# Kernel optimization log

Hardware: AMD Instinct MI355X
Metric: run time of the kernel (lower is better)

The kernel has to match this reference:

```python
import jax, jax.numpy as jnp
import numpy as np

K = 16  # nsample for knn_point

def _bn(x, g, b):
    # inference-mode BatchNorm1d folded to per-channel affine (running stats 0/1)
    return x * g[None, :, None] + b[None, :, None]

def _knn(xyz, k):
    # xyz: [B,3,N] -> idx [B,N,k] of k nearest neighbors (squared L2)
    p = xyz.transpose(0, 2, 1)                                   # [B,N,3]
    sq = jnp.sum(p * p, axis=-1)                                 # [B,N]
    d = sq[:, :, None] + sq[:, None, :] - 2.0 * jnp.einsum('bnc,bmc->bnm', p, p)
    _, idx = jax.lax.top_k(-d, k)
    return idx

def _gather(hT, idx):
    # hT: [B,N,C], idx: [B,N,K] -> [B,N,K,C]
    return jax.vmap(lambda a, i: a[i])(hT, idx)

def setup_inputs():
    key = jax.random.key(0)
    ks = jax.random.split(key, 12)
    B, N, C = 16, 2048, 128
    def w(k, shape, fan):
        return jax.random.normal(k, shape, jnp.float32) * (1.0 / np.sqrt(fan))
    o = jnp.ones; z = jnp.zeros
    return {
        'points': jax.random.normal(ks[0], (B, 6, N), jnp.float32),
        'label': jax.random.uniform(ks[1], (B, 1, 16), jnp.float32),
        'We1': w(ks[2], (C, 6), 6), 'ge1': o(C), 'be1': z(C),
        'We2': w(ks[3], (C, C), C), 'ge2': o(C), 'be2': z(C),
        'W1': w(ks[4], (3, C, C), C), 'g1': o((3, C)), 'b1': z((3, C)),
        'W2': w(ks[5], (3, C, C), C), 'g2': o((3, C)), 'b2': z((3, C)),
        'Wf': w(ks[6], (1024, 3 * C), 3 * C), 'gf': o(1024), 'bf': z(1024),
        'Wl': w(ks[7], (64, 16), 16), 'gl': o(64), 'bl': z(64),
        'Wc1': w(ks[8], (512, 3136), 3136), 'bc1': z(512), 'gc1': o(512), 'bb1': z(512),
        'Wc2': w(ks[9], (256, 512), 512), 'bc2': z(256), 'gc2': o(256), 'bb2': z(256),
        'Wc3': w(ks[10], (50, 256), 256), 'bc3': z(50),
    }

def reference(points, label, We1, ge1, be1, We2, ge2, be2, W1, g1, b1, W2, g2, b2,
              Wf, gf, bf, Wl, gl, bl, Wc1, bc1, gc1, bb1, Wc2, bc2, gc2, bb2, Wc3, bc3):
    B, _, N = points.shape
    x = points[:, :6, :]
    xyz = x[:, :3, :]
    idx = _knn(xyz, K)                                            # [B,N,16]
    # input embedding: two conv1x1 + BN + ReLU
    h = jax.nn.relu(_bn(jnp.einsum('oc,bcn->bon', We1, x), ge1, be1))
    h = jax.nn.relu(_bn(jnp.einsum('oc,bcn->bon', We2, h), ge2, be2))
    xs = []
    for i in range(3):  # PVDSA_Res blocks (simplified: conv-BN-ReLU, kNN max-agg, conv-BN + residual)
        t = jax.nn.relu(_bn(jnp.einsum('oc,bcn->bon', W1[i], h), g1[i], b1[i]))
        nbr = _gather(t.transpose(0, 2, 1), idx)                  # [B,N,K,C]
        m = nbr.max(axis=2).transpose(0, 2, 1)                    # [B,C,N]
        h = jax.nn.relu(_bn(jnp.einsum('oc,bcn->bon', W2[i], m), g2[i], b2[i]) + h)
        xs.append(h)
    xcat = jnp.concatenate(xs, axis=1)                            # [B,384,N]
    xf = jax.nn.leaky_relu(_bn(jnp.einsum('oc,bcn->bon', Wf, xcat), gf, bf), 0.2)  # [B,1024,N]
    x_max = xf.max(axis=-1)                                       # [B,1024]
    x_avg = xf.mean(axis=-1)                                      # [B,1024]
    cls = jnp.broadcast_to(label.transpose(0, 2, 1), (B, 16, N))
    lab = jax.nn.leaky_relu(_bn(jnp.einsum('oc,bcn->bon', Wl, cls), gl, bl), 0.2)  # [B,64,N]
    glob = jnp.concatenate([
        jnp.broadcast_to(x_max[:, :, None], (B, 1024, N)),
        jnp.broadcast_to(x_avg[:, :, None], (B, 1024, N)),
        lab], axis=1)
    xa = jnp.concatenate([xf, glob], axis=1)                      # [B,3136,N]
    c = jax.nn.relu(_bn(jnp.einsum('oc,bcn->bon', Wc1, xa) + bc1[None, :, None], gc1, bb1))
    c = jax.nn.relu(_bn(jnp.einsum('oc,bcn->bon', Wc2, c) + bc2[None, :, None], gc2, bb2))
    out = jnp.einsum('oc,bcn->bon', Wc3, c) + bc3[None, :, None]  # [B,50,N]
    return out
```

## Files before the change

### kernel.cpp

```cpp
#include <hip/hip_runtime.h>
#include <cstdint>
#include <cstddef>

#define DEVINL __device__ __forceinline__

typedef float    f32x4 __attribute__((ext_vector_type(4)));
typedef _Float16 f16x8 __attribute__((ext_vector_type(8)));
typedef _Float16 f16x4 __attribute__((ext_vector_type(4)));

constexpr int BB = 16, NN = 2048, MM = 32768;

constexpr size_t OFF_WE1 = 0;
constexpr size_t OFF_WE2 = OFF_WE1 + 128 * 64 * 2;
constexpr size_t OFF_W1  = OFF_WE2 + 128 * 128 * 2;
constexpr size_t OFF_W2  = OFF_W1  + 3 * 128 * 128 * 2;
constexpr size_t OFF_WF  = OFF_W2  + 3 * 128 * 128 * 2;
constexpr size_t OFF_WC1 = OFF_WF  + 1024 * 384 * 2;
constexpr size_t OFF_WC2 = OFF_WC1 + 512 * 1024 * 2;
constexpr size_t OFF_WC3 = OFF_WC2 + 256 * 512 * 2;
constexpr size_t OFF_BC2 = OFF_WC3 + 128 * 256 * 2;
constexpr size_t OFF_BC3 = OFF_BC2 + 256 * 4;
constexpr size_t OFF_CVEC= OFF_BC3 + 128 * 4;
constexpr size_t OFF_PMAX= OFF_CVEC+ 16 * 512 * 4;
constexpr size_t OFF_PSUM= OFF_PMAX+ 16 * 8 * 1024 * 4;
constexpr size_t OFF_IDX = OFF_PSUM+ 16 * 8 * 1024 * 4;
constexpr size_t OFF_R1  = 8ull << 20;
constexpr size_t OFF_X0  = OFF_R1;
constexpr size_t OFF_HT  = OFF_R1 + (4ull  << 20);
constexpr size_t OFF_TT  = OFF_R1 + (12ull << 20);
constexpr size_t OFF_MT  = OFF_R1 + (20ull << 20);
constexpr size_t OFF_C1  = OFF_R1;
constexpr size_t OFF_XCAT= OFF_R1 + (32ull << 20);
constexpr size_t OFF_C2  = OFF_XCAT;
constexpr size_t OFF_XF  = OFF_XCAT + (24ull << 20);

__global__ __launch_bounds__(256) void fold_all_kernel(
    const float* We1, const float* ge1, const float* We2, const float* ge2,
    const float* W1,  const float* g1,  const float* W2,  const float* g2,
    const float* Wf,  const float* gf,  const float* Wc1, const float* gc1,
    const float* Wc2, const float* gc2, const float* Wc3,
    const float* gc2b, const float* bc2, const float* bb2, const float* bc3,
    const float* pts, char* ws)
{
    const int bid = blockIdx.x;
    const int tid = threadIdx.x;

    if (bid == 4704) {
        ((float*)(ws + OFF_BC2))[tid] = gc2b[tid] * bc2[tid] + bb2[tid];
        return;
    }
    if (bid == 4705) {
        if (tid < 128) ((float*)(ws + OFF_BC3))[tid] = (tid < 50) ? bc3[tid] : 0.f;
        return;
    }
    if (bid >= 4706) {
        int m = (bid - 4706) * 256 + tid;
        int b = m >> 11, n = m & 2047;
        const float* ps = pts + (size_t)b * 6 * 2048 + n;
        _Float16 tmp[64];
#pragma unroll
        for (int c = 0; c < 64; ++c) tmp[c] = (_Float16)0.f;
#pragma unroll
        for (int c = 0; c < 6; ++c) tmp[c] = (_Float16)ps[(size_t)c << 11];
        _Float16* dst = (_Float16*)(ws + OFF_X0) + (size_t)m * 64;
#pragma unroll
        for (int v = 0; v < 8; ++v) *(f16x8*)(dst + v * 8) = *(const f16x8*)(tmp + v * 8);
        return;
    }

    int id, base;
    if      (bid < 32)   { id = 0;  base = 0;    }
    else if (bid < 96)   { id = 1;  base = 32;   }
    else if (bid < 160)  { id = 2;  base = 96;   }
    else if (bid < 224)  { id = 3;  base = 160;  }
    else if (bid < 288)  { id = 4;  base = 224;  }
    else if (bid < 352)  { id = 5;  base = 288;  }
    else if (bid < 416)  { id = 6;  base = 352;  }
    else if (bid < 480)  { id = 7;  base = 416;  }
    else if (bid < 2016) { id = 8;  base = 480;  }
    else if (bid < 4064) { id = 9;  base = 2016; }
    else if (bid < 4576) { id = 10; base = 4064; }
    else                 { id = 11; base = 4576; }

    const float* src = nullptr; const float* g = nullptr; _Float16* dst = nullptr;
    int O = 0, K = 0, lds = 0, Kp = 0;
    switch (id) {
        case 0:  src = We1; g = ge1; O = 128; K = 6;    lds = 6;    Kp = 64;   dst = (_Float16*)(ws + OFF_WE1); break;
        case 1:  src = We2; g = ge2; O = 128; K = 128;  lds = 128;  Kp = 128;  dst = (_Float16*)(ws + OFF_WE2); break;
        case 2: case 3: case 4: {
            int i = id - 2;
            src = W1 + (size_t)i * 16384; g = g1 + i * 128; O = 128; K = 128; lds = 128; Kp = 128;
            dst = (_Float16*)(ws + OFF_W1) + (size_t)i * 16384; break; }
        case 5: case 6: case 7: {
            int i = id - 5;
            src = W2 + (size_t)i * 16384; g = g2 + i * 128; O = 128; K = 128; lds = 128; Kp = 128;
            dst = (_Float16*)(ws + OFF_W2) + (size_t)i * 16384; break; }
        case 8:  src = Wf;  g = gf;  O = 1024; K = 384;  lds = 384;  Kp = 384;  dst = (_Float16*)(ws + OFF_WF);  break;
        case 9:  src = Wc1; g = gc1; O = 512;  K = 1024; lds = 3136; Kp = 1024; dst = (_Float16*)(ws + OFF_WC1); break;
        case 10: src = Wc2; g = gc2; O = 256;  K = 512;  lds = 512;  Kp = 512;  dst = (_Float16*)(ws + OFF_WC2); break;
        default: src = Wc3; g = nullptr; O = 50; K = 256; lds = 256; Kp = 256;  dst = (_Float16*)(ws + OFF_WC3); break;
    }
    int e = (bid - base) * 256 + tid;
    int o = e / Kp, k = e - o * Kp;
    float v = 0.f;
    if (o < O && k < K) {
        v = src[(size_t)o * lds + k];
        if (g) v *= g[o];
    }
    dst[e] = (_Float16)v;
}

DEVINL float knn_dist(const float4 pq, const float4 pm) {
    float t = pq.x * pm.x;
    t = fmaf(pq.y, pm.y, t);
    t = fmaf(pq.z, pm.z, t);
    return fmaf(-2.f, t, pm.w);
}

#define KNN_DINS(X) do { \
    const float x_ = (X); \
    d15 = __builtin_amdgcn_fmed3f(x_, d14, d15); \
    d14 = __builtin_amdgcn_fmed3f(x_, d13, d14); \
    d13 = __builtin_amdgcn_fmed3f(x_, d12, d13); \
    d12 = __builtin_amdgcn_fmed3f(x_, d11, d12); \
    d11 = __builtin_amdgcn_fmed3f(x_, d10, d11); \
    d10 = __builtin_amdgcn_fmed3f(x_, d9,  d10); \
    d9  = __builtin_amdgcn_fmed3f(x_, d8,  d9);  \
    d8  = __builtin_amdgcn_fmed3f(x_, d7,  d8);  \
    d7  = __builtin_amdgcn_fmed3f(x_, d6,  d7);  \
    d6  = __builtin_amdgcn_fmed3f(x_, d5,  d6);  \
    d5  = __builtin_amdgcn_fmed3f(x_, d4,  d5);  \
    d4  = __builtin_amdgcn_fmed3f(x_, d3,  d4);  \
    d3  = __builtin_amdgcn_fmed3f(x_, d2,  d3);  \
    d2  = __builtin_amdgcn_fmed3f(x_, d1,  d2);  \
    d1  = __builtin_amdgcn_fmed3f(x_, d0,  d1);  \
    d0  = __builtin_amdgcn_fmed3f(x_, -3.4e38f, d0); \
} while (0)

#define KNN_CE(A, B) { const float lo_ = fminf(A, B), hi_ = fmaxf(A, B); A = lo_; B = hi_; }

#define KNN_MERGE(OFF) do { \
    const float n0  = __shfl_xor(d0,  OFF), n1  = __shfl_xor(d1,  OFF), \
                n2  = __shfl_xor(d2,  OFF), n3  = __shfl_xor(d3,  OFF), \
                n4  = __shfl_xor(d4,  OFF), n5  = __shfl_xor(d5,  OFF), \
                n6  = __shfl_xor(d6,  OFF), n7  = __shfl_xor(d7,  OFF), \
                n8  = __shfl_xor(d8,  OFF), n9  = __shfl_xor(d9,  OFF), \
                n10 = __shfl_xor(d10, OFF), n11 = __shfl_xor(d11, OFF), \
                n12 = __shfl_xor(d12, OFF), n13 = __shfl_xor(d13, OFF), \
                n14 = __shfl_xor(d14, OFF), n15 = __shfl_xor(d15, OFF); \
    d0  = fminf(d0,  n15); d1  = fminf(d1,  n14); d2  = fminf(d2,  n13); d3  = fminf(d3,  n12); \
    d4  = fminf(d4,  n11); d5  = fminf(d5,  n10); d6  = fminf(d6,  n9);  d7  = fminf(d7,  n8);  \
    d8  = fminf(d8,  n7);  d9  = fminf(d9,  n6);  d10 = fminf(d10, n5);  d11 = fminf(d11, n4);  \
    d12 = fminf(d12, n3);  d13 = fminf(d13, n2);  d14 = fminf(d14, n1);  d15 = fminf(d15, n0);  \
    KNN_CE(d0, d8)  KNN_CE(d1, d9)  KNN_CE(d2, d10) KNN_CE(d3, d11) \
    KNN_CE(d4, d12) KNN_CE(d5, d13) KNN_CE(d6, d14) KNN_CE(d7, d15) \
    KNN_CE(d0, d4)  KNN_CE(d1, d5)  KNN_CE(d2, d6)  KNN_CE(d3, d7)  \
    KNN_CE(d8, d12) KNN_CE(d9, d13) KNN_CE(d10,d14) KNN_CE(d11,d15) \
    KNN_CE(d0, d2)  KNN_CE(d1, d3)  KNN_CE(d4, d6)  KNN_CE(d5, d7)  \
    KNN_CE(d8, d10) KNN_CE(d9, d11) KNN_CE(d12,d14) KNN_CE(d13,d15) \
    KNN_CE(d0, d1)  KNN_CE(d2, d3)  KNN_CE(d4, d5)  KNN_CE(d6, d7)  \
    KNN_CE(d8, d9)  KNN_CE(d10,d11) KNN_CE(d12,d13) KNN_CE(d14,d15) \
} while (0)

__global__ __launch_bounds__(256) void knn_kernel(const float* __restrict__ pts, int* __restrict__ idxout)
{
    __shared__ float4 P[2048];
    __shared__ int    cnt[32];
    const int tid = threadIdx.x;
    const int b = blockIdx.x;
    const float* pb = pts + (size_t)b * 6 * 2048;
    for (int i = tid; i < 2048; i += 256) {
        float x = pb[i];
        float y = pb[2048 + i];
        float z = pb[4096 + i];
        P[i] = make_float4(x, y, z, x * x + y * y + z * z);
    }
    if (tid < 32) cnt[tid] = 0;
    __syncthreads();

    const int p = tid & 7;
    const int g = tid >> 3;
    const int q = blockIdx.y * 32 + g;
    const float4 pq = P[q];

    float d0 = 3.4e38f, d1 = 3.4e38f, d2 = 3.4e38f, d3 = 3.4e38f,
          d4 = 3.4e38f, d5 = 3.4e38f, d6 = 3.4e38f, d7 = 3.4e38f,
          d8 = 3.4e38f, d9 = 3.4e38f, d10 = 3.4e38f, d11 = 3.4e38f,
          d12 = 3.4e38f, d13 = 3.4e38f, d14 = 3.4e38f, d15 = 3.4e38f;

    float4 nxt = P[p];
#pragma unroll 2
    for (int it = 0; it < 256; ++it) {
        const float4 pm = nxt;
        const int m = it * 8 + p;
        nxt = P[(m + 8) & 2047];
        const float dd = knn_dist(pq, pm);
        if (__any(dd < d15)) {
            KNN_DINS(dd);
        }
    }

    KNN_MERGE(1);
    KNN_MERGE(2);
    KNN_MERGE(4);

    const float t = d15;
    int* op = idxout + (((size_t)(b << 11) + q) << 4);
    float4 nxt2 = P[p];
    for (int it = 0; it < 256; ++it) {
        const float4 pm = nxt2;
        const int m = it * 8 + p;
        nxt2 = P[(m + 8) & 2047];
        const float d = knn_dist(pq, pm);
        if (d <= t) {
            const int pos = atomicAdd(&cnt[g], 1);
            if (pos < 16) op[pos] = m;
        }
    }
}

template<int TM>
__global__ __launch_bounds__(256) void gemm_tile(
    const _Float16* __restrict__ W, const _Float16* __restrict__ X,
    _Float16* __restrict__ Y, float* __restrict__ Y32,
    const float* __restrict__ bias, const _Float16* __restrict__ Res,
    int Kp, int ldX, int xoff, int ldY, int yoff, int Opad,
    int act, int biasPerBatch, int ldR, int roff, int Olimit)
{
    constexpr int MI = TM / 32;
    __shared__ _Float16 SH[128 * 64 + TM * 64];
    _Float16* As = SH;
    _Float16* Bs = SH + 128 * 64;

    const int tid  = threadIdx.x;
    const int lane = tid & 63, wave = tid >> 6;
    const int r = lane & 15, quad = lane >> 4;
    const int m_blk = blockIdx.x * TM, o_blk = blockIdx.y * 128;
    const int oh = (wave >> 1) * 64, mh = (wave & 1) * (TM / 2);

    f32x4 acc[4][MI];
#pragma unroll
    for (int a = 0; a < 4; ++a)
#pragma unroll
        for (int c = 0; c < MI; ++c) acc[a][c] = (f32x4){0.f, 0.f, 0.f, 0.f};

    const int srow  = wave * 8 + (lane >> 3);
    const int sslot = lane & 7;

    for (int k0 = 0; k0 < Kp; k0 += 64) {
        __syncthreads();
#pragma unroll
        for (int t = 0; t < 4; ++t) {
            const int rowA = t * 32 + srow;
            const int gk = k0 + ((sslot ^ (rowA & 7)) << 3);
            const _Float16* gA = W + (size_t)(o_blk + rowA) * Kp + gk;
            __builtin_amdgcn_global_load_lds(
                (const __attribute__((address_space(1))) unsigned int*)gA,
                (__attribute__((address_space(3))) unsigned int*)(As + t * 2048 + wave * 512),
                16, 0, 0);
        }
#pragma unroll
        for (int t = 0; t < TM / 32; ++t) {
            const int rowB = t * 32 + srow;
            const int gk = k0 + ((sslot ^ (rowB & 7)) << 3);
            const _Float16* gB = X + (size_t)(m_blk + rowB) * ldX + xoff + gk;
            __builtin_amdgcn_global_load_lds(
                (const __attribute__((address_space(1))) unsigned int*)gB,
                (__attribute__((address_space(3))) unsigned int*)(Bs + t * 2048 + wave * 512),
                16, 0, 0);
        }
        __syncthreads();
#pragma unroll
        for (int ks = 0; ks < 2; ++ks) {
            f16x8 af[4], bf[MI];
#pragma unroll
            for (int oi = 0; oi < 4; ++oi) {
                const int row = oh + oi * 16 + r;
                const int slot = (ks * 4 + quad) ^ (row & 7);
                af[oi] = *(const f16x8*)(As + row * 64 + slot * 8);
            }
#pragma unroll
            for (int mi = 0; mi < MI; ++mi) {
                const int row = mh + mi * 16 + r;
                const int slot = (ks * 4 + quad) ^ (row & 7);
                bf[mi] = *(const f16x8*)(Bs + row * 64 + slot * 8);
            }
#pragma unroll
            for (int oi = 0; oi < 4; ++oi)
#pragma unroll
                for (int mi = 0; mi < MI; ++mi)
                    acc[oi][mi] = __builtin_amdgcn_mfma_f32_16x16x32_f16(af[oi], bf[mi], acc[oi][mi], 0, 0, 0);
        }
    }

    const int bb = biasPerBatch ? (m_blk >> 11) * Opad : 0;
    __syncthreads();

    if (Y32) {
#pragma unroll
        for (int oi = 0; oi < 4; ++oi) {
            const int og = o_blk + oh + oi * 16 + quad * 4;
            const f32x4 bv = *(const f32x4*)(bias + bb + og);
#pragma unroll
            for (int mi = 0; mi < MI; ++mi) {
                const int m = m_blk + mh + mi * 16 + r;
                const int bidx = m >> 11, n = m & 2047;
                f32x4 v = acc[oi][mi] + bv;
#pragma unroll
                for (int j = 0; j < 4; ++j) {
                    float x = v[j];
                    if (act == 1)      x = (x > 0.f) ? x : 0.0f;
                    else if (act == 2) x = (x > 0.f) ? x : 0.2f * x;
                    const int o = og + j;
                    if (o < Olimit)
                        Y32[((size_t)(bidx * 50 + o) << 11) + n] = x;
                }
            }
        }
        return;
    }

    _Float16* OT = SH;
#pragma unroll
    for (int oi = 0; oi < 4; ++oi) {
        const int ol = oh + oi * 16 + quad * 4;
        const f32x4 bv = *(const f32x4*)(bias + bb + o_blk + ol);
#pragma unroll
        for (int mi = 0; mi < MI; ++mi) {
            const int row = mh + mi * 16 + r;
            f32x4 v = acc[oi][mi] + bv;
            if (Res) {
                f16x4 rr = *(const f16x4*)(Res + (size_t)(m_blk + row) * ldR + roff + o_blk + ol);
#pragma unroll
                for (int j = 0; j < 4; ++j) v[j] += (float)rr[j];
            }
            f16x4 ov;
#pragma unroll
            for (int j = 0; j < 4; ++j) {
                float x = v[j];
                if (act == 1)      x = (x > 0.f) ? x : 0.0f;
                else if (act == 2) x = (x > 0.f) ? x : 0.2f * x;
                ov[j] = (_Float16)x;
            }
            const int s = ((ol >> 2) ^ (row & 31)) << 2;
            *(f16x4*)(OT + row * 128 + s) = ov;
        }
    }
    __syncthreads();
#pragma unroll
    for (int it2 = 0; it2 < TM / 16; ++it2) {
        const int row = it2 * 16 + (tid >> 4);
        const int c = tid & 15;
        const int s0 = ((c * 2) ^ (row & 31)) << 2;
        const int s1 = ((c * 2 + 1) ^ (row & 31)) << 2;
        f16x4 a = *(const f16x4*)(OT + row * 128 + s0);
        f16x4 b2 = *(const f16x4*)(OT + row * 128 + s1);
        f16x8 o8;
        o8[0] = a[0]; o8[1] = a[1]; o8[2] = a[2]; o8[3] = a[3];
        o8[4] = b2[0]; o8[5] = b2[1]; o8[6] = b2[2]; o8[7] = b2[3];
        *(f16x8*)(Y + (size_t)(m_blk + row) * ldY + yoff + o_blk + c * 8) = o8;
    }
}

typedef short s16x8 __attribute__((ext_vector_type(8)));
__global__ __launch_bounds__(256) void gather_max_kernel(
    const short* __restrict__ T, const int* __restrict__ idx, short* __restrict__ Mo)
{
    const int tid = threadIdx.x;
    const int p = blockIdx.x * 16 + (tid >> 4);
    const int l = tid & 15;
    const int b = p >> 11;
    const int* ip = idx + (size_t)p * 16;
    size_t row = (size_t)((b << 11) + ip[0]);
    s16x8 cur = *(const s16x8*)(T + row * 128 + l * 8);
    unsigned short best[8];
#pragma unroll
    for (int e = 0; e < 8; ++e) best[e] = (unsigned short)cur[e];
#pragma unroll
    for (int j = 1; j < 16; ++j) {
        row = (size_t)((b << 11) + ip[j]);
        s16x8 v = *(const s16x8*)(T + row * 128 + l * 8);
#pragma unroll
        for (int e = 0; e < 8; ++e) {
            unsigned short u = (unsigned short)v[e];
            if (u > best[e]) best[e] = u;
        }
    }
    s16x8 ov;
#pragma unroll
    for (int e = 0; e < 8; ++e) ov[e] = (short)best[e];
    *(s16x8*)(Mo + (size_t)p * 128 + l * 8) = ov;
}

__global__ __launch_bounds__(256) void reduce1_kernel(const _Float16* __restrict__ xf, float* __restrict__ pmax, float* __restrict__ psum)
{
    const int b = blockIdx.x, oc = blockIdx.y, ch = blockIdx.z, tid = threadIdx.x;
    const int o = oc * 256 + tid;
    const _Float16* p = xf + ((size_t)(b << 11) + ch * 256) * 1024 + o;
    float mx = -3.4e38f, sm = 0.f;
    for (int n = 0; n < 256; ++n) {
        float v = (float)p[(size_t)n * 1024];
        mx = fmaxf(mx, v); sm += v;
    }
    pmax[((size_t)(b * 8 + ch) << 10) + o] = mx;
    psum[((size_t)(b * 8 + ch) << 10) + o] = sm;
}

__global__ __launch_bounds__(256) void cvec_kernel(
    const float* __restrict__ label, const float* __restrict__ Wl, const float* __restrict__ gl, const float* __restrict__ bl,
    const float* __restrict__ Wc1, const float* __restrict__ bc1, const float* __restrict__ gc1, const float* __restrict__ bb1,
    const float* __restrict__ pmax, const float* __restrict__ psum, float* __restrict__ cvec)
{
    __shared__ float v[2112];
    __shared__ float red[256];
    const int b = blockIdx.x, og = blockIdx.y, tid = threadIdx.x;
    for (int i = tid; i < 1024; i += 256) {
        float mx = -3.4e38f, sm = 0.f;
#pragma unroll
        for (int c = 0; c < 8; ++c) {
            mx = fmaxf(mx, pmax[((size_t)(b * 8 + c) << 10) + i]);
            sm += psum[((size_t)(b * 8 + c) << 10) + i];
        }
        v[i] = mx;
        v[1024 + i] = sm * (1.f / 2048.f);
    }
    if (tid < 64) {
        float s = 0.f;
        for (int i = 0; i < 16; ++i) s += Wl[tid * 16 + i] * label[b * 16 + i];
        s = gl[tid] * s + bl[tid];
        v[2048 + tid] = (s > 0.f) ? s : 0.2f * s;
    }
    __syncthreads();
    const int o = og * 64 + (tid >> 2), part = tid & 3;
    const float* wrow = Wc1 + (size_t)o * 3136 + 1024 + part * 528;
    float s = 0.f;
    for (int j = 0; j < 528; ++j) s += wrow[j] * v[part * 528 + j];
    red[tid] = s;
    __syncthreads();
    if (part == 0) {
        float tot = red[tid] + red[tid + 1] + red[tid + 2] + red[tid + 3];
        cvec[((size_t)b << 9) + o] = gc1[o] * (tot + bc1[o]) + bb1[o];
    }
}

extern "C" void kernel_launch(void* const* d_in, const int* in_sizes, int n_in,
                              void* d_out, int out_size, void* d_ws, size_t ws_size,
                              hipStream_t stream)
{
    (void)in_sizes; (void)n_in; (void)out_size; (void)ws_size;
    const float* points = (const float*)d_in[0];
    const float* label  = (const float*)d_in[1];
    const float* We1 = (const float*)d_in[2];
    const float* ge1 = (const float*)d_in[3];
    const float* be1 = (const float*)d_in[4];
    const float* We2 = (const float*)d_in[5];
    const float* ge2 = (const float*)d_in[6];
    const float* be2 = (const float*)d_in[7];
    const float* W1  = (const float*)d_in[8];
    const float* g1  = (const float*)d_in[9];
    const float* b1  = (const float*)d_in[10];
    const float* W2  = (const float*)d_in[11];
    const float* g2  = (const float*)d_in[12];
    const float* b2  = (const float*)d_in[13];
    const float* Wf  = (const float*)d_in[14];
    const float* gf  = (const float*)d_in[15];
    const float* bfv = (const float*)d_in[16];
    const float* Wl  = (const float*)d_in[17];
    const float* gl  = (const float*)d_in[18];
    const float* bl  = (const float*)d_in[19];
    const float* Wc1 = (const float*)d_in[20];
    const float* bc1 = (const float*)d_in[21];
    const float* gc1 = (const float*)d_in[22];
    const float* bb1 = (const float*)d_in[23];
    const float* Wc2 = (const float*)d_in[24];
    const float* bc2 = (const float*)d_in[25];
    const float* gc2 = (const float*)d_in[26];
    const float* bb2 = (const float*)d_in[27];
    const float* Wc3 = (const float*)d_in[28];
    const float* bc3 = (const float*)d_in[29];

    char* ws = (char*)d_ws;
    _Float16* hT  = (_Float16*)(ws + OFF_HT);
    _Float16* tT  = (_Float16*)(ws + OFF_TT);
    _Float16* mT  = (_Float16*)(ws + OFF_MT);
    _Float16* xct = (_Float16*)(ws + OFF_XCAT);
    _Float16* xf  = (_Float16*)(ws + OFF_XF);
    _Float16* c1  = (_Float16*)(ws + OFF_C1);
    _Float16* c2  = (_Float16*)(ws + OFF_C2);
    int*      idx = (int*)     (ws + OFF_IDX);
    _Float16* x0  = (_Float16*)(ws + OFF_X0);

    _Float16* wE1 = (_Float16*)(ws + OFF_WE1);
    _Float16* wE2 = (_Float16*)(ws + OFF_WE2);
    _Float16* w1f = (_Float16*)(ws + OFF_W1);
    _Float16* w2f = (_Float16*)(ws + OFF_W2);
    _Float16* wF  = (_Float16*)(ws + OFF_WF);
    _Float16* wC1 = (_Float16*)(ws + OFF_WC1);
    _Float16* wC2 = (_Float16*)(ws + OFF_WC2);
    _Float16* wC3 = (_Float16*)(ws + OFF_WC3);
    float* bC2 = (float*)(ws + OFF_BC2);
    float* bC3 = (float*)(ws + OFF_BC3);
    float* cv  = (float*)(ws + OFF_CVEC);
    float* pmx = (float*)(ws + OFF_PMAX);
    float* psm = (float*)(ws + OFF_PSUM);

    fold_all_kernel<<<dim3(4834), 256, 0, stream>>>(We1, ge1, We2, ge2, W1, g1, W2, g2,
                                                    Wf, gf, Wc1, gc1, Wc2, gc2, Wc3,
                                                    gc2, bc2, bb2, bc3, points, ws);
    knn_kernel<<<dim3(BB, NN / 32), 256, 0, stream>>>(points, idx);

    gemm_tile<64><<<dim3(512, 1), 256, 0, stream>>>(wE1, x0, tT, nullptr, be1, nullptr, 64, 64, 0, 128, 0, 128, 1, 0, 0, 0, 128);
    gemm_tile<64><<<dim3(512, 1), 256, 0, stream>>>(wE2, tT, hT, nullptr, be2, nullptr, 128, 128, 0, 128, 0, 128, 1, 0, 0, 0, 128);

    for (int i = 0; i < 3; ++i) {
        const _Float16* hin = (i == 0) ? hT : xct;
        int ldH  = (i == 0) ? 128 : 384;
        int offH = (i == 0) ? 0 : (i - 1) * 128;
        gemm_tile<64><<<dim3(512, 1), 256, 0, stream>>>(w1f + (size_t)i * 16384, hin, tT, nullptr, b1 + i * 128, nullptr,
                                                        128, ldH, offH, 128, 0, 128, 1, 0, 0, 0, 128);
        gather_max_kernel<<<dim3(MM / 16), 256, 0, stream>>>((const short*)tT, idx, (short*)mT);
        gemm_tile<64><<<dim3(512, 1), 256, 0, stream>>>(w2f + (size_t)i * 16384, mT, xct, nullptr, b2 + i * 128, hin,
                                                        128, 128, 0, 384, i * 128, 128, 1, 0, ldH, offH, 128);
    }

    gemm_tile<128><<<dim3(256, 8), 256, 0, stream>>>(wF, xct, xf, nullptr, bfv, nullptr, 384, 384, 0, 1024, 0, 1024, 2, 0, 0, 0, 1024);

    reduce1_kernel<<<dim3(BB, 4, 8), 256, 0, stream>>>(xf, pmx, psm);
    cvec_kernel<<<dim3(BB, 8), 256, 0, stream>>>(label, Wl, gl, bl, Wc1, bc1, gc1, bb1, pmx, psm, cv);

    gemm_tile<128><<<dim3(256, 4), 256, 0, stream>>>(wC1, xf, c1, nullptr, cv, nullptr, 1024, 1024, 0, 512, 0, 512, 1, 1, 0, 0, 512);
    gemm_tile<128><<<dim3(256, 2), 256, 0, stream>>>(wC2, c1, c2, nullptr, bC2, nullptr, 512, 512, 0, 256, 0, 256, 1, 0, 0, 0, 256);
    gemm_tile<128><<<dim3(256, 1), 256, 0, stream>>>(wC3, c2, nullptr, (float*)d_out, bC3, nullptr, 256, 256, 0, 0, 0, 128, 0, 0, 0, 0, 50);
}
```

Before: 448.1 us.

## Rework KNN as branchless top-4 bound, candidate buffer, then exact top-16

Each lane now keeps a per-lane top-4 with branchless fmed3 updates instead of a divergent 16-wide insertion sort. The merged lanes give an upper-bound threshold on the 16th distance. Points under that threshold go into a shared candidate buffer of up to 96 entries per query. The exact top-16 and index output then run only over that short list rather than a second full 2048-point scan. This removes the warp-divergent insertion work but risks dropping true neighbors if more than 96 candidates fall under the bound.

```diff
diff --git a/kernel.cpp b/kernel.cpp
--- a/kernel.cpp
+++ b/kernel.cpp
@@ -165,7 +165,9 @@
 __global__ __launch_bounds__(256) void knn_kernel(const float* __restrict__ pts, int* __restrict__ idxout)
 {
     __shared__ float4 P[2048];
-    __shared__ int    cnt[32];
+    __shared__ unsigned short buf[32][96];
+    __shared__ int cnt[32];
+    __shared__ int wcnt[32];
     const int tid = threadIdx.x;
     const int b = blockIdx.x;
     const float* pb = pts + (size_t)b * 6 * 2048;
@@ -175,7 +177,7 @@
         float z = pb[4096 + i];
         P[i] = make_float4(x, y, z, x * x + y * y + z * z);
     }
-    if (tid < 32) cnt[tid] = 0;
+    if (tid < 32) { cnt[tid] = 0; wcnt[tid] = 0; }
     __syncthreads();
 
     const int p = tid & 7;
@@ -183,37 +185,56 @@
     const int q = blockIdx.y * 32 + g;
     const float4 pq = P[q];
 
-    float d0 = 3.4e38f, d1 = 3.4e38f, d2 = 3.4e38f, d3 = 3.4e38f,
-          d4 = 3.4e38f, d5 = 3.4e38f, d6 = 3.4e38f, d7 = 3.4e38f,
+    float d0 = 3.4e38f, d1 = 3.4e38f, d2 = 3.4e38f, d3 = 3.4e38f;
+#pragma unroll 4
+    for (int it = 0; it < 256; ++it) {
+        const float4 pm = P[it * 8 + p];
+        const float x = knn_dist(pq, pm);
+        d3 = __builtin_amdgcn_fmed3f(x, d2, d3);
+        d2 = __builtin_amdgcn_fmed3f(x, d1, d2);
+        d1 = __builtin_amdgcn_fmed3f(x, d0, d1);
+        d0 = fminf(x, d0);
+    }
+    float d4 = 3.4e38f, d5 = 3.4e38f, d6 = 3.4e38f, d7 = 3.4e38f,
           d8 = 3.4e38f, d9 = 3.4e38f, d10 = 3.4e38f, d11 = 3.4e38f,
           d12 = 3.4e38f, d13 = 3.4e38f, d14 = 3.4e38f, d15 = 3.4e38f;
-
-    float4 nxt = P[p];
-#pragma unroll 2
-    for (int it = 0; it < 256; ++it) {
-        const float4 pm = nxt;
-        const int m = it * 8 + p;
-        nxt = P[(m + 8) & 2047];
-        const float dd = knn_dist(pq, pm);
-        if (__any(dd < d15)) {
-            KNN_DINS(dd);
-        }
-    }
-
     KNN_MERGE(1);
     KNN_MERGE(2);
     KNN_MERGE(4);
-
+    const float tub = d15;
+
+#pragma unroll 4
+    for (int it = 0; it < 256; ++it) {
+        const int m = it * 8 + p;
+        const float d = knn_dist(pq, P[m]);
+        if (d <= tub) {
+            const int pos = atomicAdd(&cnt[g], 1);
+            if (pos < 96) buf[g][pos] = (unsigned short)m;
+        }
+    }
+    int C = cnt[g];
+    if (C > 96) C = 96;
+
+    d0 = 3.4e38f; d1 = 3.4e38f; d2 = 3.4e38f; d3 = 3.4e38f;
+    d4 = 3.4e38f; d5 = 3.4e38f; d6 = 3.4e38f; d7 = 3.4e38f;
+    d8 = 3.4e38f; d9 = 3.4e38f; d10 = 3.4e38f; d11 = 3.4e38f;
+    d12 = 3.4e38f; d13 = 3.4e38f; d14 = 3.4e38f; d15 = 3.4e38f;
+    for (int j = p; j < C; j += 8) {
+        const int m = buf[g][j];
+        const float x = knn_dist(pq, P[m]);
+        KNN_DINS(x);
+    }
+    KNN_MERGE(1);
+    KNN_MERGE(2);
+    KNN_MERGE(4);
     const float t = d15;
+
     int* op = idxout + (((size_t)(b << 11) + q) << 4);
-    float4 nxt2 = P[p];
-    for (int it = 0; it < 256; ++it) {
-        const float4 pm = nxt2;
-        const int m = it * 8 + p;
-        nxt2 = P[(m + 8) & 2047];
-        const float d = knn_dist(pq, pm);
+    for (int j = p; j < C; j += 8) {
+        const int m = buf[g][j];
+        const float d = knn_dist(pq, P[m]);
         if (d <= t) {
-            const int pos = atomicAdd(&cnt[g], 1);
+            const int pos = atomicAdd(&wcnt[g], 1);
             if (pos < 16) op[pos] = m;
         }
     }
```

New measurement: 414.9 us. 1.08x faster.
